# Kernel tuning notes

Hardware: AMD Instinct MI355X
Metric: run time of the kernel (lower is better)

The kernel has to match this reference:

```python
import jax, jax.numpy as jnp
import numpy as np

D_MODEL = 512
NUM_EXPERTS = 8
TOP_K = 2
FFN = 2048
H = 2 * D_MODEL            # GRU hidden per direction
GRU_OUT = 4 * D_MODEL      # bidirectional concat
B, T = 8, 1024
BAL_W, Z_W = 0.01, 0.001


def setup_inputs() -> dict:
    key = jax.random.key(0)
    ks = jax.random.split(key, 12)
    s = 1.0 / np.sqrt(H)  # torch GRU uniform init scale
    u = lambda k, shape: jax.random.uniform(k, shape, jnp.float32, -s, s)
    tn = lambda k, shape: jax.random.normal(k, shape, jnp.float32) * 0.02
    return {
        "x": jax.random.normal(ks[0], (B, T, D_MODEL), jnp.float32),
        # GRU params, stacked [2 directions, ...]; gate order (r, z, n) as in torch
        "gru_Wih": u(ks[1], (2, 3 * H, D_MODEL)),
        "gru_Whh": u(ks[2], (2, 3 * H, H)),
        "gru_bih": u(ks[3], (2, 3 * H)),
        "gru_bhh": u(ks[4], (2, 3 * H)),
        "gate_W": tn(ks[5], (NUM_EXPERTS, GRU_OUT)),
        "gate_b": jnp.zeros((NUM_EXPERTS,), jnp.float32),
        "W1": tn(ks[6], (NUM_EXPERTS, GRU_OUT, FFN)),
        "b1": jnp.zeros((NUM_EXPERTS, FFN), jnp.float32),
        "W2": tn(ks[7], (NUM_EXPERTS, FFN, D_MODEL)),
        "b2": jnp.zeros((NUM_EXPERTS, D_MODEL), jnp.float32),
    }


def _gru_bidir(x, Wih, Whh, bih, bhh):
    # x: [B,T,D]; returns [B,T,2H]
    Bn = x.shape[0]

    def run(d, reverse):
        # precompute input projections: [T,B,3H]
        xg = jnp.swapaxes(jnp.einsum('btd,gd->btg', x, Wih[d]) + bih[d], 0, 1)
        Whh_d, bhh_d = Whh[d], bhh[d]

        def step(h, xt):
            hg = h @ Whh_d.T + bhh_d
            xr, xz, xn = jnp.split(xt, 3, axis=-1)
            hr, hz, hn = jnp.split(hg, 3, axis=-1)
            r = jax.nn.sigmoid(xr + hr)
            z = jax.nn.sigmoid(xz + hz)
            n = jnp.tanh(xn + r * hn)
            h_new = (1.0 - z) * n + z * h
            return h_new, h_new

        h0 = jnp.zeros((Bn, H), x.dtype)
        _, ys = jax.lax.scan(step, h0, xg, reverse=reverse)  # ys[t] aligned with time t
        return jnp.swapaxes(ys, 0, 1)

    return jnp.concatenate([run(0, False), run(1, True)], axis=-1)


def reference(x, gru_Wih, gru_Whh, gru_bih, gru_bhh, gate_W, gate_b, W1, b1, W2, b2):
    Bn, Tn, _ = x.shape
    n = Bn * Tn
    E = NUM_EXPERTS

    gru_out = _gru_bidir(x, gru_Wih, gru_Whh, gru_bih, gru_bhh)
    gru_out = jax.nn.leaky_relu(gru_out, 0.01)          # dropout=0.0 -> identity
    flat = gru_out.reshape(n, GRU_OUT)

    # gating (expert_bias buffer is zeros at init)
    logits = flat @ gate_W.T + gate_b                    # [n,E]
    z_loss = Z_W * jnp.mean(jnp.square(jax.nn.logsumexp(logits, axis=-1)))
    scores = jax.nn.softmax(logits, axis=-1)
    top_scores, top_idx = jax.lax.top_k(scores, TOP_K)   # [n,K]
    weights = top_scores / jnp.sum(top_scores, axis=-1, keepdims=True)

    expert_mask = jnp.sum(jax.nn.one_hot(top_idx, E, dtype=jnp.float32), axis=1)  # [n,E]
    f = jax.lax.stop_gradient(jnp.mean(expert_mask, axis=0))
    P = jnp.mean(scores, axis=0)
    balance_loss = BAL_W * E * jnp.sum(f * P)
    aux_loss = balance_loss + z_loss

    # masked-dense expert combine (math identical to gather/scatter loop)
    output = jnp.zeros((n, D_MODEL), jnp.float32)
    for e in range(E):
        h = jax.nn.gelu(flat @ W1[e] + b1[e], approximate=False)  # [n,FFN]
        out_e = h @ W2[e] + b2[e]                                 # [n,D]
        w_e = jnp.sum(weights * (top_idx == e), axis=-1)          # [n]
        output = output + w_e[:, None] * out_e

    return output.reshape(Bn, Tn, D_MODEL).astype(x.dtype), aux_loss
```

## Files before the change

kernel.cpp:

```cpp
#include <hip/hip_runtime.h>
#include <math.h>

#define NTOK 8192
#define DM   512
#define HID  1024
#define G3H  3072
#define GOUT 2048
#define FFND 2048
#define NEXP 8

typedef float f32x4 __attribute__((ext_vector_type(4)));

#define XG_OFF    0ULL
#define HG_OFF    0ULL
#define OG_OFF    134217728ULL
#define FLAT_OFF  201326592ULL
#define HBUF_OFF  268435456ULL
#define FLAGS_OFF 268566528ULL
#define IMETA_OFF 268567552ULL
#define FMETA_OFF 268571648ULL
#define TKIDX_OFF 268575744ULL
#define TKW_OFF   268641280ULL
#define PAIRT_OFF 268706816ULL
#define PAIRW_OFF 268772352ULL
#define SLOT_OFF  268837888ULL

__global__ void k0_init(unsigned* p) {
    int i = blockIdx.x * 256 + threadIdx.x;
    if (i < 32768) p[i] = (unsigned)((i >> 13) & 1);
    else if (i < 35072) p[i] = 0u;
}

__global__ __launch_bounds__(256, 2) void k1_sgemm_bt(
    const float* __restrict__ A, const float* __restrict__ B,
    const float* __restrict__ bias, float* __restrict__ C) {
    __shared__ float As[16 * 132];
    __shared__ float Bs[16 * 132];
    const int tid = threadIdx.x;
    const int m0 = blockIdx.y * 128;
    const int n0 = blockIdx.x * 128;
    const int tx = tid & 15, ty = tid >> 4;
    const int arow = tid >> 2, ac4 = (tid & 3) * 4;
    float acc[8][8];
#pragma unroll
    for (int i = 0; i < 8; ++i)
#pragma unroll
        for (int j = 0; j < 8; ++j) acc[i][j] = 0.f;

    for (int k0 = 0; k0 < 512; k0 += 16) {
        __syncthreads();
#pragma unroll
        for (int r = 0; r < 2; ++r) {
            int row = r * 64 + arow;
            float4 va = *(const float4*)(A + (size_t)(m0 + row) * 512 + k0 + ac4);
            As[(ac4 + 0) * 132 + row] = va.x;
            As[(ac4 + 1) * 132 + row] = va.y;
            As[(ac4 + 2) * 132 + row] = va.z;
            As[(ac4 + 3) * 132 + row] = va.w;
            float4 vb = *(const float4*)(B + (size_t)(n0 + row) * 512 + k0 + ac4);
            Bs[(ac4 + 0) * 132 + row] = vb.x;
            Bs[(ac4 + 1) * 132 + row] = vb.y;
            Bs[(ac4 + 2) * 132 + row] = vb.z;
            Bs[(ac4 + 3) * 132 + row] = vb.w;
        }
        __syncthreads();
#pragma unroll
        for (int k = 0; k < 16; ++k) {
            float4 a0 = *(const float4*)&As[k * 132 + ty * 8];
            float4 a1 = *(const float4*)&As[k * 132 + ty * 8 + 4];
            float4 b0 = *(const float4*)&Bs[k * 132 + tx * 8];
            float4 b1 = *(const float4*)&Bs[k * 132 + tx * 8 + 4];
            float av[8] = {a0.x, a0.y, a0.z, a0.w, a1.x, a1.y, a1.z, a1.w};
            float bv[8] = {b0.x, b0.y, b0.z, b0.w, b1.x, b1.y, b1.z, b1.w};
#pragma unroll
            for (int i = 0; i < 8; ++i)
#pragma unroll
                for (int j = 0; j < 8; ++j) acc[i][j] = fmaf(av[i], bv[j], acc[i][j]);
        }
    }
    float4 c0 = *(const float4*)(bias + n0 + tx * 8);
    float4 c1 = *(const float4*)(bias + n0 + tx * 8 + 4);
    float bb[8] = {c0.x, c0.y, c0.z, c0.w, c1.x, c1.y, c1.z, c1.w};
#pragma unroll
    for (int i = 0; i < 8; ++i) {
        float* op = C + (size_t)(m0 + ty * 8 + i) * 6144 + n0 + tx * 8;
        float4 o0 = make_float4(acc[i][0] + bb[0], acc[i][1] + bb[1],
                                acc[i][2] + bb[2], acc[i][3] + bb[3]);
        float4 o1 = make_float4(acc[i][4] + bb[4], acc[i][5] + bb[5],
                                acc[i][6] + bb[6], acc[i][7] + bb[7]);
        *(float4*)op = o0;
        *(float4*)(op + 4) = o1;
    }
}

__global__ __launch_bounds__(256) void k2_gru(
    const float* __restrict__ Whh, const float* __restrict__ bhh,
    const float* __restrict__ xg, float* __restrict__ flat,
    float* hbuf, int* flags) {
    __shared__ float hlsf[8192];
    __shared__ float red[64 * 196];
    __shared__ float s2b[192];
    char* hls = (char*)hlsf;
    const int tid = threadIdx.x;
    const int dir = blockIdx.x >> 7;
    const int wg = blockIdx.x & 127;
    const int j0 = wg << 3;
    float* hb = hbuf + dir * 16384;
    int* fl = flags + dir * 128;
    const int rg = tid & 3;
    const int kc = tid >> 2;
    const int wv = tid >> 6;
    const int lane = tid & 63;
    const int xr16 = (kc & 15) << 4;

    const float* W0 = Whh + (size_t)dir * G3H * HID;
    float wreg[6][16];
#pragma unroll
    for (int rr = 0; rr < 6; ++rr) {
        const int r = rg * 6 + rr;
        const float* wp = W0 + (size_t)(((r >> 3) << 10) + j0 + (r & 7)) * 1024 + (kc << 4);
        const float4 w0 = ((const float4*)wp)[0];
        const float4 w1 = ((const float4*)wp)[1];
        const float4 w2 = ((const float4*)wp)[2];
        const float4 w3 = ((const float4*)wp)[3];
        wreg[rr][0] = w0.x;  wreg[rr][1] = w0.y;  wreg[rr][2] = w0.z;  wreg[rr][3] = w0.w;
        wreg[rr][4] = w1.x;  wreg[rr][5] = w1.y;  wreg[rr][6] = w1.z;  wreg[rr][7] = w1.w;
        wreg[rr][8] = w2.x;  wreg[rr][9] = w2.y;  wreg[rr][10] = w2.z; wreg[rr][11] = w2.w;
        wreg[rr][12] = w3.x; wreg[rr][13] = w3.y; wreg[rr][14] = w3.z; wreg[rr][15] = w3.w;
    }
    float bhh_r = 0.f;
    if (tid < 192) {
        const int r = tid >> 3;
        bhh_r = bhh[dir * G3H + ((r >> 3) << 10) + j0 + (r & 7)];
    }
    const int u = tid >> 3, bb = tid & 7;
    float hprev = 0.f;

    for (int s = 1; s <= 1024; ++s) {
        const int te = dir ? (1024 - s) : (s - 1);
        float xr = 0.f, xz = 0.f, xn = 0.f;
        if (tid < 64) {
            const float* xp = xg + (size_t)((bb << 10) + te) * 6144 + dir * G3H + j0 + u;
            xr = xp[0];
            xz = xp[1024];
            xn = xp[2048];
        }
        const float* hp = hb + (((s - 1) & 1) << 13);
        const unsigned expb = (((unsigned)(s - 1)) >> 1) & 1u;
        if (s > 1) {
            const int c0 = s - 1;
            int it = 0;
            for (;;) {
                int f = __hip_atomic_load(fl + (wv << 5) + (lane & 31),
                                          __ATOMIC_RELAXED, __HIP_MEMORY_SCOPE_AGENT);
                if (__all(f >= c0)) break;
                if (++it > (1 << 20)) break;
                __builtin_amdgcn_s_sleep(1);
            }
        }
        asm volatile("" ::: "memory");
        const float* hbase = hp + (wv << 11) + (lane << 2);
        f32x4 hv4[8];
        {
            int it2 = 0;
            for (;;) {
#pragma unroll
                for (int c = 0; c < 8; ++c)
                    asm volatile("global_load_dwordx4 %0, %1, off sc0 sc1"
                                 : "=v"(hv4[c]) : "v"(hbase + (c << 8)));
                asm volatile("s_waitcnt vmcnt(0)" ::: "memory");
                __builtin_amdgcn_sched_barrier(0);
                unsigned bad = 0u;
#pragma unroll
                for (int c = 0; c < 8; ++c) {
                    bad |= (__float_as_uint(hv4[c].x) ^ expb);
                    bad |= (__float_as_uint(hv4[c].y) ^ expb);
                    bad |= (__float_as_uint(hv4[c].z) ^ expb);
                    bad |= (__float_as_uint(hv4[c].w) ^ expb);
                }
                if (__all((bad & 1u) == 0u)) break;
                if (++it2 > (1 << 16)) break;
                __builtin_amdgcn_s_sleep(1);
            }
        }
#pragma unroll
        for (int c = 0; c < 8; ++c) {
            const int off = (wv << 13) +
                ((((c << 10) + (lane << 4))) ^ ((((c << 1) | (lane >> 5)) & 15) << 4));
            *(f32x4*)(hls + off) = hv4[c];
        }
        asm volatile("s_waitcnt lgkmcnt(0)" ::: "memory");
        __builtin_amdgcn_sched_barrier(0);
        const int rbase = wv << 13;
        float acc[6][8];
#pragma unroll
        for (int rr = 0; rr < 6; ++rr)
#pragma unroll
            for (int q = 0; q < 8; ++q) acc[rr][q] = 0.f;
#pragma unroll
        for (int i = 0; i < 16; ++i) {
            const int k_local = ((kc & 15) << 4) + i;
            const int a0 = rbase + ((k_local << 5) ^ xr16);
            const float4 hA = *(const float4*)(hls + a0);
            const float4 hB = *(const float4*)(hls + (a0 ^ 16));
#pragma unroll
            for (int rr = 0; rr < 6; ++rr) {
                const float w = wreg[rr][i];
                acc[rr][0] = fmaf(w, hA.x, acc[rr][0]);
                acc[rr][1] = fmaf(w, hA.y, acc[rr][1]);
                acc[rr][2] = fmaf(w, hA.z, acc[rr][2]);
                acc[rr][3] = fmaf(w, hA.w, acc[rr][3]);
                acc[rr][4] = fmaf(w, hB.x, acc[rr][4]);
                acc[rr][5] = fmaf(w, hB.y, acc[rr][5]);
                acc[rr][6] = fmaf(w, hB.z, acc[rr][6]);
                acc[rr][7] = fmaf(w, hB.w, acc[rr][7]);
            }
        }
        float* rp = red + kc * 196 + rg * 48;
#pragma unroll
        for (int rr = 0; rr < 6; ++rr) {
            *(float4*)(rp + (rr << 3)) =
                make_float4(acc[rr][0], acc[rr][1], acc[rr][2], acc[rr][3]);
            *(float4*)(rp + (rr << 3) + 4) =
                make_float4(acc[rr][4], acc[rr][5], acc[rr][6], acc[rr][7]);
        }
        __syncthreads();
        if (tid < 192) {
            float a0 = 0.f, a1 = 0.f, a2 = 0.f, a3 = 0.f;
#pragma unroll
            for (int q = 0; q < 64; q += 4) {
                a0 += red[(q + 0) * 196 + tid];
                a1 += red[(q + 1) * 196 + tid];
                a2 += red[(q + 2) * 196 + tid];
                a3 += red[(q + 3) * 196 + tid];
            }
            s2b[tid] = (a0 + a1) + (a2 + a3) + bhh_r;
        }
        __syncthreads();
        if (tid < 64) {
            const float hr = s2b[tid];
            const float hz = s2b[64 + tid];
            const float hn = s2b[128 + tid];
            const float rg_ = 1.f / (1.f + expf(-(xr + hr)));
            const float zg_ = 1.f / (1.f + expf(-(xz + hz)));
            const float ng_ = tanhf(xn + rg_ * hn);
            const float hnew = (1.f - zg_) * ng_ + zg_ * hprev;
            hprev = hnew;
            const unsigned hu = (__float_as_uint(hnew) & ~1u) | (((unsigned)s >> 1) & 1u);
            __hip_atomic_store(hb + ((s & 1) << 13) + ((j0 + u) << 3) + bb,
                               __uint_as_float(hu),
                               __ATOMIC_RELAXED, __HIP_MEMORY_SCOPE_AGENT);
            asm volatile("" ::: "memory");
            if (tid == 0)
                __hip_atomic_store(fl + wg, s, __ATOMIC_RELAXED, __HIP_MEMORY_SCOPE_AGENT);
            const float lr = hnew > 0.f ? hnew : 0.01f * hnew;
            flat[(size_t)((bb << 10) + te) * 2048 + dir * 1024 + j0 + u] = lr;
        }
    }
}

__global__ __launch_bounds__(256) void k3_gate(
    const float* __restrict__ flat, const float* __restrict__ gate_W,
    const float* __restrict__ gate_b,
    int* __restrict__ tk_idx, float* __restrict__ tk_w,
    int* __restrict__ counts, float* __restrict__ fmeta) {
    __shared__ float gw[8 * 2048];
    __shared__ float bP[9];
    __shared__ int bC[8];
    const int tid = threadIdx.x;
    for (int i = tid; i < 8 * 2048; i += 256) gw[i] = gate_W[i];
    if (tid < 9) bP[tid] = 0.f;
    if (tid < 8) bC[tid] = 0;
    __syncthreads();
    const int lane = tid & 63, w = tid >> 6;
    const int tbase = blockIdx.x * 16 + w * 4;
    for (int j = 0; j < 4; ++j) {
        int t = tbase + j;
        const float* fr = flat + (size_t)t * 2048;
        float a[8];
#pragma unroll
        for (int e = 0; e < 8; ++e) a[e] = 0.f;
        for (int i = 0; i < 32; ++i) {
            float v = fr[i * 64 + lane];
#pragma unroll
            for (int e = 0; e < 8; ++e) a[e] = fmaf(v, gw[e * 2048 + i * 64 + lane], a[e]);
        }
#pragma unroll
        for (int e = 0; e < 8; ++e) {
#pragma unroll
            for (int off = 32; off > 0; off >>= 1) a[e] += __shfl_down(a[e], off);
        }
        if (lane == 0) {
            float lg[8];
#pragma unroll
            for (int e = 0; e < 8; ++e) lg[e] = a[e] + gate_b[e];
            float m = lg[0];
#pragma unroll
            for (int e = 1; e < 8; ++e) m = fmaxf(m, lg[e]);
            float sc[8], ssum = 0.f;
#pragma unroll
            for (int e = 0; e < 8; ++e) { sc[e] = expf(lg[e] - m); ssum += sc[e]; }
            float inv = 1.f / ssum;
#pragma unroll
            for (int e = 0; e < 8; ++e) sc[e] *= inv;
            float lse = m + logf(ssum);
            int i1 = 0; float s1 = sc[0];
#pragma unroll
            for (int e = 1; e < 8; ++e) if (sc[e] > s1) { s1 = sc[e]; i1 = e; }
            int i2 = (i1 == 0) ? 1 : 0; float s2v = sc[i2];
#pragma unroll
            for (int e = 0; e < 8; ++e) if (e != i1 && sc[e] > s2v) { s2v = sc[e]; i2 = e; }
            float wsum = s1 + s2v;
            tk_idx[2 * t] = i1; tk_idx[2 * t + 1] = i2;
            tk_w[2 * t] = s1 / wsum; tk_w[2 * t + 1] = s2v / wsum;
            atomicAdd(&bC[i1], 1);
            atomicAdd(&bC[i2], 1);
#pragma unroll
            for (int e = 0; e < 8; ++e) atomicAdd(&bP[e], sc[e]);
            atomicAdd(&bP[8], lse * lse);
        }
    }
    __syncthreads();
    if (tid < 8) {
        atomicAdd(&counts[tid], bC[tid]);
        atomicAdd(&fmeta[tid], bP[tid]);
    }
    if (tid == 8) atomicAdd(&fmeta[8], bP[8]);
}

__global__ void k4_sched(int* im, float* fm, float* aux_out) {
    int tid = threadIdx.x;
    if (tid < 136) { im[32 + tid] = -1; im[168 + tid] = 0; }
    __syncthreads();
    if (tid == 0) {
        int off = 0;
        for (int e = 0; e < 8; ++e) { im[16 + e] = off; im[8 + e] = off; off += im[e]; }
        im[24] = off;
        int T = 0;
        for (int e = 0; e < 8; ++e) {
            int c = im[e], o = im[16 + e];
            for (int i = 0; i < c; i += 128) { im[32 + T] = e; im[168 + T] = o + i; ++T; }
        }
        im[25] = T;
        float fP = 0.f;
        for (int e = 0; e < 8; ++e) fP += ((float)im[e] / 8192.f) * (fm[e] / 8192.f);
        *aux_out = 0.01f * 8.f * fP + 0.001f * (fm[8] / 8192.f);
    }
}

__global__ __launch_bounds__(256) void k5_scatter(
    const int* __restrict__ tk_idx, const float* __restrict__ tk_w,
    int* __restrict__ im, int* __restrict__ pair_t,
    float* __restrict__ pair_w, int* __restrict__ slot) {
    __shared__ int cnt[8], base[8];
    const int tid = threadIdx.x;
    if (tid < 8) cnt[tid] = 0;
    __syncthreads();
    const int t = blockIdx.x * 256 + tid;
    const int e0 = tk_idx[2 * t], e1 = tk_idx[2 * t + 1];
    const int p0 = atomicAdd(&cnt[e0], 1);
    const int p1 = atomicAdd(&cnt[e1], 1);
    __syncthreads();
    if (tid < 8) base[tid] = atomicAdd(&im[8 + tid], cnt[tid]);
    __syncthreads();
    const int q0 = base[e0] + p0, q1 = base[e1] + p1;
    pair_t[q0] = t; pair_w[q0] = tk_w[2 * t];     slot[2 * t] = q0;
    pair_t[q1] = t; pair_w[q1] = tk_w[2 * t + 1]; slot[2 * t + 1] = q1;
}

__global__ __launch_bounds__(256, 2) void k6_ffn1(
    const float* __restrict__ flat, const float* __restrict__ W1,
    const float* __restrict__ b1, const int* __restrict__ im,
    const int* __restrict__ pair_t, float* __restrict__ Hg) {
    const int rt = blockIdx.x % 136;
    const int nt = blockIdx.x / 136;
    const int e = im[32 + rt];
    if (e < 0) return;
    const int pStart = im[168 + rt];
    const int pEnd = im[16 + e + 1];
    __shared__ float As[16 * 132];
    __shared__ float Bs[16 * 132];
    const int tid = threadIdx.x;
    const int tx = tid & 15, ty = tid >> 4;
    const int n0 = nt * 128;
    const float* Bb = W1 + (size_t)e * 2048 * 2048;
    const int arow = tid >> 2, ac4 = (tid & 3) * 4;
    const int bk = tid >> 4, bn = (tid & 15) * 8;
    int r0 = pStart + arow;       if (r0 > pEnd - 1) r0 = pEnd - 1;
    int r1 = pStart + 64 + arow;  if (r1 > pEnd - 1) r1 = pEnd - 1;
    const float* arp0 = flat + (size_t)pair_t[r0] * 2048;
    const float* arp1 = flat + (size_t)pair_t[r1] * 2048;
    float acc[8][8];
#pragma unroll
    for (int i = 0; i < 8; ++i)
#pragma unroll
        for (int j = 0; j < 8; ++j) acc[i][j] = 0.f;

    for (int k0 = 0; k0 < 2048; k0 += 16) {
        __syncthreads();
        {
            float4 va = *(const float4*)(arp0 + k0 + ac4);
            As[(ac4 + 0) * 132 + arow] = va.x;
            As[(ac4 + 1) * 132 + arow] = va.y;
            As[(ac4 + 2) * 132 + arow] = va.z;
            As[(ac4 + 3) * 132 + arow] = va.w;
            float4 vb = *(const float4*)(arp1 + k0 + ac4);
            As[(ac4 + 0) * 132 + 64 + arow] = vb.x;
            As[(ac4 + 1) * 132 + 64 + arow] = vb.y;
            As[(ac4 + 2) * 132 + 64 + arow] = vb.z;
            As[(ac4 + 3) * 132 + 64 + arow] = vb.w;
            float4 w0 = *(const float4*)(Bb + (size_t)(k0 + bk) * 2048 + n0 + bn);
            float4 w1 = *(const float4*)(Bb + (size_t)(k0 + bk) * 2048 + n0 + bn + 4);
            *(float4*)&Bs[bk * 132 + bn] = w0;
            *(float4*)&Bs[bk * 132 + bn + 4] = w1;
        }
        __syncthreads();
#pragma unroll
        for (int k = 0; k < 16; ++k) {
            float4 a0 = *(const float4*)&As[k * 132 + ty * 8];
            float4 a1 = *(const float4*)&As[k * 132 + ty * 8 + 4];
            float4 b0 = *(const float4*)&Bs[k * 132 + tx * 8];
            float4 b1v = *(const float4*)&Bs[k * 132 + tx * 8 + 4];
            float av[8] = {a0.x, a0.y, a0.z, a0.w, a1.x, a1.y, a1.z, a1.w};
            float bv[8] = {b0.x, b0.y, b0.z, b0.w, b1v.x, b1v.y, b1v.z, b1v.w};
#pragma unroll
            for (int i = 0; i < 8; ++i)
#pragma unroll
                for (int j = 0; j < 8; ++j) acc[i][j] = fmaf(av[i], bv[j], acc[i][j]);
        }
    }
    float4 c0 = *(const float4*)(b1 + (size_t)e * 2048 + n0 + tx * 8);
    float4 c1 = *(const float4*)(b1 + (size_t)e * 2048 + n0 + tx * 8 + 4);
    float bb[8] = {c0.x, c0.y, c0.z, c0.w, c1.x, c1.y, c1.z, c1.w};
#pragma unroll
    for (int i = 0; i < 8; ++i) {
        int p = pStart + ty * 8 + i;
        if (p < pEnd) {
            float* op = Hg + (size_t)p * 2048 + n0 + tx * 8;
            float o[8];
#pragma unroll
            for (int j = 0; j < 8; ++j) {
                float xv = acc[i][j] + bb[j];
                o[j] = 0.5f * xv * (1.f + erff(xv * 0.70710678118654752f));
            }
            *(float4*)op = make_float4(o[0], o[1], o[2], o[3]);
            *(float4*)(op + 4) = make_float4(o[4], o[5], o[6], o[7]);
        }
    }
}

__global__ __launch_bounds__(256, 2) void k7_ffn2(
    const float* __restrict__ Hg, const float* __restrict__ W2,
    const float* __restrict__ b2, const int* __restrict__ im,
    float* __restrict__ Og) {
    const int rt = blockIdx.x % 136;
    const int nt = blockIdx.x / 136;
    const int e = im[32 + rt];
    if (e < 0) return;
    const int pStart = im[168 + rt];
    const int pEnd = im[16 + e + 1];
    __shared__ float As[16 * 132];
    __shared__ float Bs[16 * 132];
    const int tid = threadIdx.x;
    const int tx = tid & 15, ty = tid >> 4;
    const int n0 = nt * 128;
    const float* Bb = W2 + (size_t)e * 2048 * 512;
    const int arow = tid >> 2, ac4 = (tid & 3) * 4;
    const int bk = tid >> 4, bn = (tid & 15) * 8;
    int r0 = pStart + arow;       if (r0 > pEnd - 1) r0 = pEnd - 1;
    int r1 = pStart + 64 + arow;  if (r1 > pEnd - 1) r1 = pEnd - 1;
    const float* arp0 = Hg + (size_t)r0 * 2048;
    const float* arp1 = Hg + (size_t)r1 * 2048;
    float acc[8][8];
#pragma unroll
    for (int i = 0; i < 8; ++i)
#pragma unroll
        for (int j = 0; j < 8; ++j) acc[i][j] = 0.f;

    for (int k0 = 0; k0 < 2048; k0 += 16) {
        __syncthreads();
        {
            float4 va = *(const float4*)(arp0 + k0 + ac4);
            As[(ac4 + 0) * 132 + arow] = va.x;
            As[(ac4 + 1) * 132 + arow] = va.y;
            As[(ac4 + 2) * 132 + arow] = va.z;
            As[(ac4 + 3) * 132 + arow] = va.w;
            float4 vb = *(const float4*)(arp1 + k0 + ac4);
            As[(ac4 + 0) * 132 + 64 + arow] = vb.x;
            As[(ac4 + 1) * 132 + 64 + arow] = vb.y;
            As[(ac4 + 2) * 132 + 64 + arow] = vb.z;
            As[(ac4 + 3) * 132 + 64 + arow] = vb.w;
            float4 w0 = *(const float4*)(Bb + (size_t)(k0 + bk) * 512 + n0 + bn);
            float4 w1 = *(const float4*)(Bb + (size_t)(k0 + bk) * 512 + n0 + bn + 4);
            *(float4*)&Bs[bk * 132 + bn] = w0;
            *(float4*)&Bs[bk * 132 + bn + 4] = w1;
        }
        __syncthreads();
#pragma unroll
        for (int k = 0; k < 16; ++k) {
            float4 a0 = *(const float4*)&As[k * 132 + ty * 8];
            float4 a1 = *(const float4*)&As[k * 132 + ty * 8 + 4];
            float4 b0 = *(const float4*)&Bs[k * 132 + tx * 8];
            float4 b1v = *(const float4*)&Bs[k * 132 + tx * 8 + 4];
            float av[8] = {a0.x, a0.y, a0.z, a0.w, a1.x, a1.y, a1.z, a1.w};
            float bv[8] = {b0.x, b0.y, b0.z, b0.w, b1v.x, b1v.y, b1v.z, b1v.w};
#pragma unroll
            for (int i = 0; i < 8; ++i)
#pragma unroll
                for (int j = 0; j < 8; ++j) acc[i][j] = fmaf(av[i], bv[j], acc[i][j]);
        }
    }
    float4 c0 = *(const float4*)(b2 + (size_t)e * 512 + n0 + tx * 8);
    float4 c1 = *(const float4*)(b2 + (size_t)e * 512 + n0 + tx * 8 + 4);
    float bb[8] = {c0.x, c0.y, c0.z, c0.w, c1.x, c1.y, c1.z, c1.w};
#pragma unroll
    for (int i = 0; i < 8; ++i) {
        int p = pStart + ty * 8 + i;
        if (p < pEnd) {
            float* op = Og + (size_t)p * 512 + n0 + tx * 8;
            *(float4*)op = make_float4(acc[i][0] + bb[0], acc[i][1] + bb[1],
                                       acc[i][2] + bb[2], acc[i][3] + bb[3]);
            *(float4*)(op + 4) = make_float4(acc[i][4] + bb[4], acc[i][5] + bb[5],
                                             acc[i][6] + bb[6], acc[i][7] + bb[7]);
        }
    }
}

__global__ __launch_bounds__(256) void k8_comb(
    const float* __restrict__ Og, const int* __restrict__ slot,
    const float* __restrict__ pw, float* __restrict__ out) {
    const int i4 = blockIdx.x * 256 + threadIdx.x;
    const int t = i4 >> 7;
    const int d = (i4 & 127) << 2;
    const int s0 = slot[2 * t], s1 = slot[2 * t + 1];
    const float w0 = pw[s0], w1 = pw[s1];
    float4 a = *(const float4*)(Og + (size_t)s0 * 512 + d);
    float4 b = *(const float4*)(Og + (size_t)s1 * 512 + d);
    float4 o = make_float4(w0 * a.x + w1 * b.x, w0 * a.y + w1 * b.y,
                           w0 * a.z + w1 * b.z, w0 * a.w + w1 * b.w);
    *(float4*)(out + (size_t)t * 512 + d) = o;
}

extern "C" void kernel_launch(void* const* d_in, const int* in_sizes, int n_in,
                              void* d_out, int out_size, void* d_ws, size_t ws_size,
                              hipStream_t stream) {
    (void)in_sizes; (void)n_in; (void)out_size; (void)ws_size;
    const float* x   = (const float*)d_in[0];
    const float* Wih = (const float*)d_in[1];
    const float* Whh = (const float*)d_in[2];
    const float* bih = (const float*)d_in[3];
    const float* bhh = (const float*)d_in[4];
    const float* gW  = (const float*)d_in[5];
    const float* gb  = (const float*)d_in[6];
    const float* W1  = (const float*)d_in[7];
    const float* b1  = (const float*)d_in[8];
    const float* W2  = (const float*)d_in[9];
    const float* b2  = (const float*)d_in[10];
    float* out = (float*)d_out;
    char* ws = (char*)d_ws;
    float* xg    = (float*)(ws + XG_OFF);
    float* Hg    = (float*)(ws + HG_OFF);
    float* Og    = (float*)(ws + OG_OFF);
    float* flat  = (float*)(ws + FLAT_OFF);
    float* hbuf  = (float*)(ws + HBUF_OFF);
    int*   flags = (int*)(ws + FLAGS_OFF);
    int*   im    = (int*)(ws + IMETA_OFF);
    float* fm    = (float*)(ws + FMETA_OFF);
    int*   tki   = (int*)(ws + TKIDX_OFF);
    float* tkw   = (float*)(ws + TKW_OFF);
    int*   prt   = (int*)(ws + PAIRT_OFF);
    float* prw   = (float*)(ws + PAIRW_OFF);
    int*   slt   = (int*)(ws + SLOT_OFF);

    hipLaunchKernelGGL(k0_init, dim3(138), dim3(256), 0, stream, (unsigned*)(ws + HBUF_OFF));
    hipLaunchKernelGGL(k1_sgemm_bt, dim3(48, 64), dim3(256), 0, stream, x, Wih, bih, xg);
    hipLaunchKernelGGL(k2_gru, dim3(256), dim3(256), 0, stream, Whh, bhh, xg, flat, hbuf, flags);
    hipLaunchKernelGGL(k3_gate, dim3(512), dim3(256), 0, stream, flat, gW, gb, tki, tkw, im, fm);
    hipLaunchKernelGGL(k4_sched, dim3(1), dim3(256), 0, stream, im, fm, out + 4194304);
    hipLaunchKernelGGL(k5_scatter, dim3(32), dim3(256), 0, stream, tki, tkw, im, prt, prw, slt);
    hipLaunchKernelGGL(k6_ffn1, dim3(136 * 16), dim3(256), 0, stream, flat, W1, b1, im, prt, Hg);
    hipLaunchKernelGGL(k7_ffn2, dim3(136 * 4), dim3(256), 0, stream, Hg, W2, b2, im, Og);
    hipLaunchKernelGGL(k8_comb, dim3(4096), dim3(256), 0, stream, Og, slt, prw, out);
}
```

Measured before the change: 9.998 ms.

## Split GRU recurrence into per-batch chains with 64 blocks each and shuffle reductions

The persistent GRU kernel previously ran one chain per direction across 128 blocks, each handling all 8 batch rows. It now runs 16 independent chains (direction x batch) of 64 blocks, each owning 16 hidden units and a 12x16 register tile of Whh. Each chain step reads only a 1024-float hidden state, and the partial dot products are reduced with wave shuffles instead of a large LDS reduction buffer. The intent is to shrink per-step sync traffic and latency and to spread work over more CUs. In exchange, every Whh slice is replicated across 8 chains, register pressure rises, and the flags now reuse the top-k index buffer, which k0 zeroes.

```diff
diff --git a/kernel.cpp b/kernel.cpp
--- a/kernel.cpp
+++ b/kernel.cpp
@@ -16,7 +16,6 @@
 #define OG_OFF    134217728ULL
 #define FLAT_OFF  201326592ULL
 #define HBUF_OFF  268435456ULL
-#define FLAGS_OFF 268566528ULL
 #define IMETA_OFF 268567552ULL
 #define FMETA_OFF 268571648ULL
 #define TKIDX_OFF 268575744ULL
@@ -25,10 +24,15 @@
 #define PAIRW_OFF 268772352ULL
 #define SLOT_OFF  268837888ULL
 
-__global__ void k0_init(unsigned* p) {
+__global__ void k0_init(char* ws) {
     int i = blockIdx.x * 256 + threadIdx.x;
-    if (i < 32768) p[i] = (unsigned)((i >> 13) & 1);
-    else if (i < 35072) p[i] = 0u;
+    if (i < 32768) {
+        ((unsigned*)(ws + HBUF_OFF))[i] = (unsigned)((i >> 10) & 1);
+    } else if (i < 33792) {
+        ((unsigned*)(ws + TKIDX_OFF))[i - 32768] = 0u;
+    } else if (i < 35840) {
+        ((unsigned*)(ws + IMETA_OFF))[i - 33792] = 0u;
+    }
 }
 
 __global__ __launch_bounds__(256, 2) void k1_sgemm_bt(
@@ -93,32 +97,32 @@
     }
 }
 
-__global__ __launch_bounds__(256) void k2_gru(
+__global__ __launch_bounds__(256, 4) void k2_gru(
     const float* __restrict__ Whh, const float* __restrict__ bhh,
     const float* __restrict__ xg, float* __restrict__ flat,
     float* hbuf, int* flags) {
-    __shared__ float hlsf[8192];
-    __shared__ float red[64 * 196];
-    __shared__ float s2b[192];
-    char* hls = (char*)hlsf;
+    __shared__ float s2c[208];
     const int tid = threadIdx.x;
-    const int dir = blockIdx.x >> 7;
-    const int wg = blockIdx.x & 127;
-    const int j0 = wg << 3;
-    float* hb = hbuf + dir * 16384;
-    int* fl = flags + dir * 128;
+    const int bid = blockIdx.x;
+    const int chain = bid >> 6;
+    const int rb = bid & 63;
+    const int dir = chain >> 3;
+    const int bat = chain & 7;
+    const int j0 = rb << 4;
     const int rg = tid & 3;
     const int kc = tid >> 2;
     const int wv = tid >> 6;
     const int lane = tid & 63;
-    const int xr16 = (kc & 15) << 4;
+    float* hb = hbuf + chain * 2048;
+    int* fl = flags + chain * 64;
 
     const float* W0 = Whh + (size_t)dir * G3H * HID;
-    float wreg[6][16];
-#pragma unroll
-    for (int rr = 0; rr < 6; ++rr) {
-        const int r = rg * 6 + rr;
-        const float* wp = W0 + (size_t)(((r >> 3) << 10) + j0 + (r & 7)) * 1024 + (kc << 4);
+    float wreg[12][16];
+#pragma unroll
+    for (int rr = 0; rr < 12; ++rr) {
+        const int r = rg * 12 + rr;
+        const int grow = ((r >> 4) << 10) + j0 + (r & 15);
+        const float* wp = W0 + (size_t)grow * 1024 + (kc << 4);
         const float4 w0 = ((const float4*)wp)[0];
         const float4 w1 = ((const float4*)wp)[1];
         const float4 w2 = ((const float4*)wp)[2];
@@ -128,134 +132,119 @@
         wreg[rr][8] = w2.x;  wreg[rr][9] = w2.y;  wreg[rr][10] = w2.z; wreg[rr][11] = w2.w;
         wreg[rr][12] = w3.x; wreg[rr][13] = w3.y; wreg[rr][14] = w3.z; wreg[rr][15] = w3.w;
     }
-    float bhh_r = 0.f;
-    if (tid < 192) {
-        const int r = tid >> 3;
-        bhh_r = bhh[dir * G3H + ((r >> 3) << 10) + j0 + (r & 7)];
-    }
-    const int u = tid >> 3, bb = tid & 7;
+    float bh_r = 0.f, bh_z = 0.f, bh_n = 0.f;
+    if (tid < 16) {
+        bh_r = bhh[dir * G3H + j0 + tid];
+        bh_z = bhh[dir * G3H + 1024 + j0 + tid];
+        bh_n = bhh[dir * G3H + 2048 + j0 + tid];
+    }
     float hprev = 0.f;
 
     for (int s = 1; s <= 1024; ++s) {
         const int te = dir ? (1024 - s) : (s - 1);
         float xr = 0.f, xz = 0.f, xn = 0.f;
-        if (tid < 64) {
-            const float* xp = xg + (size_t)((bb << 10) + te) * 6144 + dir * G3H + j0 + u;
+        if (tid < 16) {
+            const float* xp = xg + (size_t)((bat << 10) + te) * 6144 + dir * G3H + j0 + tid;
             xr = xp[0];
             xz = xp[1024];
             xn = xp[2048];
         }
-        const float* hp = hb + (((s - 1) & 1) << 13);
+        const float* hp = hb + (((s - 1) & 1) << 10);
         const unsigned expb = (((unsigned)(s - 1)) >> 1) & 1u;
         if (s > 1) {
             const int c0 = s - 1;
             int it = 0;
             for (;;) {
-                int f = __hip_atomic_load(fl + (wv << 5) + (lane & 31),
-                                          __ATOMIC_RELAXED, __HIP_MEMORY_SCOPE_AGENT);
+                int f = __hip_atomic_load(fl + lane, __ATOMIC_RELAXED, __HIP_MEMORY_SCOPE_AGENT);
                 if (__all(f >= c0)) break;
-                if (++it > (1 << 20)) break;
+                if (++it > (1 << 14)) break;
                 __builtin_amdgcn_s_sleep(1);
             }
         }
         asm volatile("" ::: "memory");
-        const float* hbase = hp + (wv << 11) + (lane << 2);
-        f32x4 hv4[8];
+        f32x4 hv;
         {
+            const float* ha = hp + (tid << 2);
             int it2 = 0;
             for (;;) {
-#pragma unroll
-                for (int c = 0; c < 8; ++c)
-                    asm volatile("global_load_dwordx4 %0, %1, off sc0 sc1"
-                                 : "=v"(hv4[c]) : "v"(hbase + (c << 8)));
+                asm volatile("global_load_dwordx4 %0, %1, off sc0 sc1"
+                             : "=v"(hv) : "v"(ha));
                 asm volatile("s_waitcnt vmcnt(0)" ::: "memory");
                 __builtin_amdgcn_sched_barrier(0);
-                unsigned bad = 0u;
-#pragma unroll
-                for (int c = 0; c < 8; ++c) {
-                    bad |= (__float_as_uint(hv4[c].x) ^ expb);
-                    bad |= (__float_as_uint(hv4[c].y) ^ expb);
-                    bad |= (__float_as_uint(hv4[c].z) ^ expb);
-                    bad |= (__float_as_uint(hv4[c].w) ^ expb);
-                }
+                unsigned bad = (__float_as_uint(hv.x) ^ expb) |
+                               (__float_as_uint(hv.y) ^ expb) |
+                               (__float_as_uint(hv.z) ^ expb) |
+                               (__float_as_uint(hv.w) ^ expb);
                 if (__all((bad & 1u) == 0u)) break;
-                if (++it2 > (1 << 16)) break;
+                if (++it2 > (1 << 12)) break;
                 __builtin_amdgcn_s_sleep(1);
             }
         }
-#pragma unroll
-        for (int c = 0; c < 8; ++c) {
-            const int off = (wv << 13) +
-                ((((c << 10) + (lane << 4))) ^ ((((c << 1) | (lane >> 5)) & 15) << 4));
-            *(f32x4*)(hls + off) = hv4[c];
-        }
-        asm volatile("s_waitcnt lgkmcnt(0)" ::: "memory");
-        __builtin_amdgcn_sched_barrier(0);
-        const int rbase = wv << 13;
-        float acc[6][8];
-#pragma unroll
-        for (int rr = 0; rr < 6; ++rr)
-#pragma unroll
-            for (int q = 0; q < 8; ++q) acc[rr][q] = 0.f;
-#pragma unroll
-        for (int i = 0; i < 16; ++i) {
-            const int k_local = ((kc & 15) << 4) + i;
-            const int a0 = rbase + ((k_local << 5) ^ xr16);
-            const float4 hA = *(const float4*)(hls + a0);
-            const float4 hB = *(const float4*)(hls + (a0 ^ 16));
-#pragma unroll
-            for (int rr = 0; rr < 6; ++rr) {
-                const float w = wreg[rr][i];
-                acc[rr][0] = fmaf(w, hA.x, acc[rr][0]);
-                acc[rr][1] = fmaf(w, hA.y, acc[rr][1]);
-                acc[rr][2] = fmaf(w, hA.z, acc[rr][2]);
-                acc[rr][3] = fmaf(w, hA.w, acc[rr][3]);
-                acc[rr][4] = fmaf(w, hB.x, acc[rr][4]);
-                acc[rr][5] = fmaf(w, hB.y, acc[rr][5]);
-                acc[rr][6] = fmaf(w, hB.z, acc[rr][6]);
-                acc[rr][7] = fmaf(w, hB.w, acc[rr][7]);
-            }
-        }
-        float* rp = red + kc * 196 + rg * 48;
-#pragma unroll
-        for (int rr = 0; rr < 6; ++rr) {
-            *(float4*)(rp + (rr << 3)) =
-                make_float4(acc[rr][0], acc[rr][1], acc[rr][2], acc[rr][3]);
-            *(float4*)(rp + (rr << 3) + 4) =
-                make_float4(acc[rr][4], acc[rr][5], acc[rr][6], acc[rr][7]);
-        }
-        __syncthreads();
-        if (tid < 192) {
-            float a0 = 0.f, a1 = 0.f, a2 = 0.f, a3 = 0.f;
-#pragma unroll
-            for (int q = 0; q < 64; q += 4) {
-                a0 += red[(q + 0) * 196 + tid];
-                a1 += red[(q + 1) * 196 + tid];
-                a2 += red[(q + 2) * 196 + tid];
-                a3 += red[(q + 3) * 196 + tid];
-            }
-            s2b[tid] = (a0 + a1) + (a2 + a3) + bhh_r;
-        }
-        __syncthreads();
-        if (tid < 64) {
-            const float hr = s2b[tid];
-            const float hz = s2b[64 + tid];
-            const float hn = s2b[128 + tid];
+        const int qb = lane & ~3;
+        f32x4 hk0, hk1, hk2, hk3;
+        hk0.x = __shfl(hv.x, qb);     hk0.y = __shfl(hv.y, qb);
+        hk0.z = __shfl(hv.z, qb);     hk0.w = __shfl(hv.w, qb);
+        hk1.x = __shfl(hv.x, qb + 1); hk1.y = __shfl(hv.y, qb + 1);
+        hk1.z = __shfl(hv.z, qb + 1); hk1.w = __shfl(hv.w, qb + 1);
+        hk2.x = __shfl(hv.x, qb + 2); hk2.y = __shfl(hv.y, qb + 2);
+        hk2.z = __shfl(hv.z, qb + 2); hk2.w = __shfl(hv.w, qb + 2);
+        hk3.x = __shfl(hv.x, qb + 3); hk3.y = __shfl(hv.y, qb + 3);
+        hk3.z = __shfl(hv.z, qb + 3); hk3.w = __shfl(hv.w, qb + 3);
+        float acc[12];
+#pragma unroll
+        for (int rr = 0; rr < 12; ++rr) {
+            float a;
+            a = wreg[rr][0] * hk0.x;
+            a = fmaf(wreg[rr][1],  hk0.y, a);
+            a = fmaf(wreg[rr][2],  hk0.z, a);
+            a = fmaf(wreg[rr][3],  hk0.w, a);
+            a = fmaf(wreg[rr][4],  hk1.x, a);
+            a = fmaf(wreg[rr][5],  hk1.y, a);
+            a = fmaf(wreg[rr][6],  hk1.z, a);
+            a = fmaf(wreg[rr][7],  hk1.w, a);
+            a = fmaf(wreg[rr][8],  hk2.x, a);
+            a = fmaf(wreg[rr][9],  hk2.y, a);
+            a = fmaf(wreg[rr][10], hk2.z, a);
+            a = fmaf(wreg[rr][11], hk2.w, a);
+            a = fmaf(wreg[rr][12], hk3.x, a);
+            a = fmaf(wreg[rr][13], hk3.y, a);
+            a = fmaf(wreg[rr][14], hk3.z, a);
+            a = fmaf(wreg[rr][15], hk3.w, a);
+            acc[rr] = a;
+        }
+#pragma unroll
+        for (int rr = 0; rr < 12; ++rr) {
+            acc[rr] += __shfl_xor(acc[rr], 4);
+            acc[rr] += __shfl_xor(acc[rr], 8);
+            acc[rr] += __shfl_xor(acc[rr], 16);
+            acc[rr] += __shfl_xor(acc[rr], 32);
+        }
+        const int kcl = kc & 15;
+#pragma unroll
+        for (int rr = 0; rr < 12; ++rr)
+            if (kcl == rr) s2c[wv * 48 + rg * 12 + rr] = acc[rr];
+        __syncthreads();
+        if (tid < 16) {
+            float hr = s2c[tid]       + s2c[48 + tid]       + s2c[96 + tid]       + s2c[144 + tid];
+            float hz = s2c[16 + tid]  + s2c[64 + tid]       + s2c[112 + tid]      + s2c[160 + tid];
+            float hn = s2c[32 + tid]  + s2c[80 + tid]       + s2c[128 + tid]      + s2c[176 + tid];
+            hr += bh_r; hz += bh_z; hn += bh_n;
             const float rg_ = 1.f / (1.f + expf(-(xr + hr)));
             const float zg_ = 1.f / (1.f + expf(-(xz + hz)));
             const float ng_ = tanhf(xn + rg_ * hn);
             const float hnew = (1.f - zg_) * ng_ + zg_ * hprev;
             hprev = hnew;
             const unsigned hu = (__float_as_uint(hnew) & ~1u) | (((unsigned)s >> 1) & 1u);
-            __hip_atomic_store(hb + ((s & 1) << 13) + ((j0 + u) << 3) + bb,
+            __hip_atomic_store(hb + ((s & 1) << 10) + j0 + tid,
                                __uint_as_float(hu),
                                __ATOMIC_RELAXED, __HIP_MEMORY_SCOPE_AGENT);
             asm volatile("" ::: "memory");
             if (tid == 0)
-                __hip_atomic_store(fl + wg, s, __ATOMIC_RELAXED, __HIP_MEMORY_SCOPE_AGENT);
+                __hip_atomic_store(fl + rb, s, __ATOMIC_RELAXED, __HIP_MEMORY_SCOPE_AGENT);
             const float lr = hnew > 0.f ? hnew : 0.01f * hnew;
-            flat[(size_t)((bb << 10) + te) * 2048 + dir * 1024 + j0 + u] = lr;
-        }
+            flat[(size_t)((bat << 10) + te) * 2048 + dir * 1024 + j0 + tid] = lr;
+        }
+        __syncthreads();
     }
 }
 
@@ -563,18 +552,18 @@
     float* Og    = (float*)(ws + OG_OFF);
     float* flat  = (float*)(ws + FLAT_OFF);
     float* hbuf  = (float*)(ws + HBUF_OFF);
-    int*   flags = (int*)(ws + FLAGS_OFF);
     int*   im    = (int*)(ws + IMETA_OFF);
     float* fm    = (float*)(ws + FMETA_OFF);
+    int*   flags = (int*)(ws + TKIDX_OFF);
     int*   tki   = (int*)(ws + TKIDX_OFF);
     float* tkw   = (float*)(ws + TKW_OFF);
     int*   prt   = (int*)(ws + PAIRT_OFF);
     float* prw   = (float*)(ws + PAIRW_OFF);
     int*   slt   = (int*)(ws + SLOT_OFF);
 
-    hipLaunchKernelGGL(k0_init, dim3(138), dim3(256), 0, stream, (unsigned*)(ws + HBUF_OFF));
+    hipLaunchKernelGGL(k0_init, dim3(140), dim3(256), 0, stream, ws);
     hipLaunchKernelGGL(k1_sgemm_bt, dim3(48, 64), dim3(256), 0, stream, x, Wih, bih, xg);
-    hipLaunchKernelGGL(k2_gru, dim3(256), dim3(256), 0, stream, Whh, bhh, xg, flat, hbuf, flags);
+    hipLaunchKernelGGL(k2_gru, dim3(1024), dim3(256), 0, stream, Whh, bhh, xg, flat, hbuf, flags);
     hipLaunchKernelGGL(k3_gate, dim3(512), dim3(256), 0, stream, flat, gW, gb, tki, tkw, im, fm);
     hipLaunchKernelGGL(k4_sched, dim3(1), dim3(256), 0, stream, im, fm, out + 4194304);
     hipLaunchKernelGGL(k5_scatter, dim3(32), dim3(256), 0, stream, tki, tkw, im, prt, prw, slt);
```

New measurement: 37.09 ms. 3.71x slower.
